# Kernel tuning notes

Measured on AMD Instinct MI355X. Metric: run time of the kernel, lower is better.

The kernel has to match this reference:

```python
import jax, jax.numpy as jnp
import numpy as np
from jax import lax

N_NODES = 8192
N_FEAT = 256
N_EDGES = 131072


def _cc_labels(src, dst, n):
    """Weakly-connected-component labels via min-label propagation + pointer jumping.
    Converged label[i] == min node index in i's component (matches scipy's
    first-occurrence labeling order after compaction)."""
    def cond(state):
        return state[1]

    def body(state):
        label, _ = state
        m = jnp.minimum(label[src], label[dst])
        new = label.at[src].min(m).at[dst].min(m)
        new = new[new]  # pointer jump
        return new, jnp.any(new != label)

    label, _ = lax.while_loop(cond, body, (jnp.arange(n, dtype=jnp.int32), jnp.array(True)))
    return label


def setup_inputs() -> dict:
    key = jax.random.key(0)
    k1, k2, k3 = jax.random.split(key, 3)
    x = jax.random.normal(k1, (N_NODES, N_FEAT), dtype=jnp.float32)
    edge_index = jax.random.randint(k2, (2, N_EDGES), 0, N_NODES, dtype=jnp.int32)
    batch = jnp.zeros((N_NODES,), dtype=jnp.int32)
    lin_w = jax.random.normal(k3, (1, 2 * N_FEAT), dtype=jnp.float32) * 0.05
    lin_b = jnp.zeros((1,), dtype=jnp.float32)
    return {"x": x, "edge_index": edge_index, "batch": batch, "lin_w": lin_w, "lin_b": lin_b}


def reference(x, edge_index, batch, lin_w, lin_b):
    n, f = x.shape
    src, dst = edge_index[0], edge_index[1]
    msk = src != dst  # drop self loops (kept in buffer, zeroed via mask for static shapes)
    # undirected: add flipped edges -> 2E directed edges
    src2 = jnp.concatenate([src, dst])
    dst2 = jnp.concatenate([dst, src])
    m2 = jnp.concatenate([msk, msk])
    mf = m2.astype(x.dtype)

    # edge score: Linear(2F,1) on [x[src] || x[dst]] == x@w1 gathered + x@w2 gathered
    w1, w2 = lin_w[0, :f], lin_w[0, f:]
    p1 = x @ w1  # [N]
    p2 = x @ w2  # [N]
    e = jnp.tanh(p1[src2] + p2[dst2] + lin_b[0])  # [2E]

    # contracted edges: score > threshold (0.0); masked edges excluded
    contract = m2 & (e > 0.0)
    srcc = jnp.where(contract, src2, 0)
    dstc = jnp.where(contract, dst2, 0)
    label = _cc_labels(srcc, dstc, n)
    # compact labels in order of smallest node index per component (== scipy ordering)
    is_root = (label == jnp.arange(n, dtype=label.dtype))
    cluster = (jnp.cumsum(is_root.astype(jnp.int32)) - 1)[label]  # [N], values in [0, K)

    # dense adjacency A and score adjacency S (scatter-add, like to_dense_adj)
    A = jnp.zeros((n, n), x.dtype).at[src2, dst2].add(mf)
    S = jnp.zeros((n, n), x.dtype).at[src2, dst2].add(e * mf)

    # isolated nodes w.r.t. contracted adjacency -> S[i,i] = 1
    cint = contract.astype(jnp.int32)
    deg = jnp.zeros(n, jnp.int32).at[src2].add(cint) + jnp.zeros(n, jnp.int32).at[dst2].add(cint)
    isolated = deg == 0
    idx = jnp.arange(n)
    S = S.at[idx, idx].set(jnp.where(isolated, jnp.ones((), x.dtype), S[idx, idx]))

    # X_new = (S @ C).T @ X = C.T @ (S.T @ X)  -- C.T@ is a segment-sum over clusters
    # (padded to N rows; rows >= num_clusters are zero)
    X_new = jax.ops.segment_sum(S.T @ x, cluster, num_segments=n)

    # coarsened adjacency C.T @ A @ C with zero diagonal (dense, padded to NxN)
    M1 = jax.ops.segment_sum(A, cluster, num_segments=n)        # pool rows
    A_c = jax.ops.segment_sum(M1.T, cluster, num_segments=n).T  # pool cols
    A_c = A_c.at[idx, idx].set(0.0)

    new_batch = jnp.zeros(n, batch.dtype).at[cluster].set(batch)
    return X_new, A_c, new_batch, cluster
```

## Files before the change

kernel.cpp:

```cpp
#include <hip/hip_runtime.h>
#include <math.h>

#define N_NODES 8192
#define N_FEAT  256
#define N_EDGES 131072
#define N_DIR   (2*N_EDGES)
#define MAXDEG  128


__device__ __forceinline__ void edge_sd(const int* __restrict__ ei, int k, int& s, int& d){
  s = ei[k];
  d = (k < N_EDGES) ? ei[k + N_EDGES] : ei[k - N_EDGES];
}


__global__ void k_zero(uint4* __restrict__ p, long long n4,
                       int* __restrict__ meta, int nmeta){
  long long i = (long long)blockIdx.x * blockDim.x + threadIdx.x;
  long long stride = (long long)gridDim.x * blockDim.x;
  uint4 z = {0u, 0u, 0u, 0u};
  for (long long k = i; k < n4; k += stride) p[k] = z;
  for (long long k = i; k < nmeta; k += stride) meta[k] = 0;
}

__global__ void k_proj(const float* __restrict__ x, const float* __restrict__ w,
                       float* __restrict__ p1, float* __restrict__ p2){
  int i = blockIdx.x;
  int t = threadIdx.x;
  float v = x[(size_t)i * N_FEAT + t];
  double a = (double)v * (double)w[t];
  double b = (double)v * (double)w[N_FEAT + t];
  for (int off = 32; off; off >>= 1){
    a += __shfl_down(a, off);
    b += __shfl_down(b, off);
  }
  __shared__ double sa[4], sb[4];
  int wid = t >> 6, lane = t & 63;
  if (lane == 0){ sa[wid] = a; sb[wid] = b; }
  __syncthreads();
  if (t == 0){
    p1[i] = (float)(sa[0] + sa[1] + sa[2] + sa[3]);
    p2[i] = (float)(sb[0] + sb[1] + sb[2] + sb[3]);
  }
}

__global__ void k_edges(const int* __restrict__ ei, const float* __restrict__ p1,
                        const float* __restrict__ p2, const float* __restrict__ lb,
                        int* __restrict__ cnt, int* __restrict__ deg,
                        uint2* __restrict__ edata,
                        unsigned int* __restrict__ pairs, int* __restrict__ np){
  int k = blockIdx.x * blockDim.x + threadIdx.x;
  int s, d; edge_sd(ei, k, s, d);
  bool selfe = (s == d);
  float e = 0.0f;
  if (!selfe){
    float z = p1[s] + p2[d] + lb[0];
    e = tanhf(z);
    int slot = atomicAdd(&cnt[d], 1);
    uint2 v; v.x = (unsigned int)s; v.y = __float_as_uint(e);
    edata[(size_t)d * MAXDEG + slot] = v;
    if (e > 0.0f){
      atomicAdd(&deg[s], 1);
      atomicAdd(&deg[d], 1);
    }
  }
  bool c = (!selfe) && (e > 0.0f);
  unsigned long long m = __ballot(c);
  if (m){
    int lane = threadIdx.x & 63;
    int leader = __ffsll((unsigned long long)m) - 1;
    int base = 0;
    if (lane == leader) base = atomicAdd(np, __popcll(m));
    base = __shfl(base, leader);
    if (c){
      int prefix = __popcll(m & ((1ull << lane) - 1ull));
      pairs[base + prefix] = ((unsigned int)s << 13) | (unsigned int)d;
    }
  }
}

__global__ void __launch_bounds__(1024) k_cc(
    const unsigned int* __restrict__ pairs, const int* __restrict__ np,
    const int* __restrict__ batch,
    int* __restrict__ cluster_i, float* __restrict__ out_cluster,
    float* __restrict__ out_batch){
  __shared__ int L[N_NODES];
  __shared__ int wsum[1024];
  __shared__ int flag;

  int t = threadIdx.x;
  for (int i = t; i < N_NODES; i += 1024) L[i] = i;
  if (t == 0) flag = 0;
  __syncthreads();

  int n = *np;
  while (true){
    for (int k = t; k < n; k += 1024){
      unsigned int p = pairs[k];
      int s = (int)(p >> 13), d = (int)(p & 8191u);
      int a = L[s], b = L[d];
      if (a == b) continue;
      int m = a < b ? a : b;
      atomicMin(&L[s], m);
      atomicMin(&L[d], m);
      if (a > m) atomicMin(&L[a], m);
      else       atomicMin(&L[b], m);
      flag = 1;
    }
    __syncthreads();
    if (!flag) break;
    for (int i = t; i < N_NODES; i += 1024){
      int l = L[i];
      while (true){ int q = L[l]; if (q == l) break; l = q; }
      L[i] = l;
    }
    __syncthreads();
    if (t == 0) flag = 0;
    __syncthreads();
  }

  int base = t * 8;
  int l_reg[8];
  #pragma unroll
  for (int j = 0; j < 8; ++j) l_reg[j] = L[base + j];
  __syncthreads();

  int f[8]; int s = 0;
  #pragma unroll
  for (int j = 0; j < 8; ++j){ f[j] = (l_reg[j] == base + j) ? 1 : 0; s += f[j]; }
  wsum[t] = s;
  __syncthreads();
  for (int off = 1; off < 1024; off <<= 1){
    int v = (t >= off) ? wsum[t - off] : 0;
    __syncthreads();
    wsum[t] += v;
    __syncthreads();
  }
  int run = wsum[t] - s;
  #pragma unroll
  for (int j = 0; j < 8; ++j){
    run += f[j];
    if (f[j]) L[base + j] = run - 1;
  }
  __syncthreads();

  #pragma unroll
  for (int j = 0; j < 8; ++j){
    int i = base + j;
    int c = L[l_reg[j]];
    cluster_i[i] = c;
    out_cluster[i] = (float)c;
    out_batch[c] = (float)batch[i];
  }
}

__global__ void k_y(const float* __restrict__ x, const uint2* __restrict__ edata,
                    const int* __restrict__ cnt, const int* __restrict__ deg,
                    float* __restrict__ y){
  int i = blockIdx.x;
  int t = threadIdx.x;
  int m = cnt[i];
  float acc = (deg[i] == 0) ? x[(size_t)i * N_FEAT + t] : 0.0f;
  const uint2* row = edata + (size_t)i * MAXDEG;
  for (int j = 0; j < m; ++j){
    uint2 v = row[j];
    acc += __uint_as_float(v.y) * x[(size_t)v.x * N_FEAT + t];
  }
  y[(size_t)i * N_FEAT + t] = acc;
}

__global__ void k_xnew(const float* __restrict__ y, const int* __restrict__ cluster_i,
                       float* __restrict__ Xn){
  int t = threadIdx.x;
  int node0 = blockIdx.x * 32;
  float acc = 0.0f;
  int cur = cluster_i[node0];
  for (int j = 0; j < 32; ++j){
    int node = node0 + j;
    int c = cluster_i[node];
    if (c != cur){
      atomicAdd(&Xn[(size_t)cur * N_FEAT + t], acc);
      acc = 0.0f; cur = c;
    }
    acc += y[(size_t)node * N_FEAT + t];
  }
  atomicAdd(&Xn[(size_t)cur * N_FEAT + t], acc);
}

__global__ void k_ac(const int* __restrict__ ei, const int* __restrict__ cluster_i,
                     float* __restrict__ Ac){
  int k = blockIdx.x * blockDim.x + threadIdx.x;
  if (k >= N_DIR) return;
  int s, d; edge_sd(ei, k, s, d);
  if (s == d) return;
  int cs = cluster_i[s], cd = cluster_i[d];
  if (cs != cd) atomicAdd(&Ac[(size_t)cs * N_NODES + cd], 1.0f);
}


extern "C" void kernel_launch(void* const* d_in, const int* in_sizes, int n_in,
                              void* d_out, int out_size, void* d_ws, size_t ws_size,
                              hipStream_t stream){
  const float* x     = (const float*)d_in[0];
  const int*   ei    = (const int*)  d_in[1];
  const int*   batch = (const int*)  d_in[2];
  const float* lw    = (const float*)d_in[3];
  const float* lb    = (const float*)d_in[4];

  float* out = (float*)d_out;
  float* Xn  = out;
  float* Ac  = Xn + (size_t)N_NODES * N_FEAT;
  float* ob  = Ac + (size_t)N_NODES * N_NODES;
  float* oc  = ob + N_NODES;

  char* w = (char*)d_ws;
  float* p1        = (float*)w; w += (size_t)N_NODES * 4;
  float* p2        = (float*)w; w += (size_t)N_NODES * 4;
  int*   cluster_i = (int*)  w; w += (size_t)N_NODES * 4;
  int*   meta      = (int*)  w;
  int*   cnt       = meta;
  int*   deg       = meta + N_NODES;
  int*   np        = meta + 2 * N_NODES;
  w += (size_t)(2 * N_NODES + 16) * 4;
  unsigned int* pairs = (unsigned int*)w; w += (size_t)N_DIR * 4;
  uint2* edata     = (uint2*)w; w += (size_t)N_NODES * MAXDEG * 8;
  float* y         = (float*)w; w += (size_t)N_NODES * N_FEAT * 4;

  long long n4 = (long long)out_size / 4;
  int nmeta = 2 * N_NODES + 16;

  k_zero  <<<4096, 256, 0, stream>>>((uint4*)d_out, n4, meta, nmeta);
  k_proj  <<<N_NODES, 256, 0, stream>>>(x, lw, p1, p2);
  k_edges <<<N_DIR / 256, 256, 0, stream>>>(ei, p1, p2, lb, cnt, deg, edata, pairs, np);
  k_cc    <<<1, 1024, 0, stream>>>(pairs, np, batch, cluster_i, oc, ob);
  k_y     <<<N_NODES, 256, 0, stream>>>(x, edata, cnt, deg, y);
  k_xnew  <<<N_NODES / 32, 256, 0, stream>>>(y, cluster_i, Xn);
  k_ac    <<<N_DIR / 256, 256, 0, stream>>>(ei, cluster_i, Ac);
}
```

Measured before the change: 269.4 us.

## Pre-relax components on whole GPU, filter active edges, overlap zeroing with CC block

Connected-component labeling now runs two grid-wide relax and flatten passes on a global label array. Only the edges still joining different labels are collected, and the single-block finisher iterates over that smaller set, staged in LDS when it fits. The big output zeroing is moved into extra blocks of the same launch as the single-block CC kernel, so it runs alongside it using nontemporal stores. This adds several small launches and could fall back to global reads when too many edges remain active.

```diff
diff --git a/kernel.cpp b/kernel.cpp
--- a/kernel.cpp
+++ b/kernel.cpp
@@ -6,6 +6,9 @@
 #define N_EDGES 131072
 #define N_DIR   (2*N_EDGES)
 #define MAXDEG  128
+#define ACT_CAP 24576
+
+typedef unsigned int u32x4 __attribute__((ext_vector_type(4)));
 
 
 __device__ __forceinline__ void edge_sd(const int* __restrict__ ei, int k, int& s, int& d){
@@ -14,13 +17,10 @@
 }
 
 
-__global__ void k_zero(uint4* __restrict__ p, long long n4,
-                       int* __restrict__ meta, int nmeta){
-  long long i = (long long)blockIdx.x * blockDim.x + threadIdx.x;
-  long long stride = (long long)gridDim.x * blockDim.x;
-  uint4 z = {0u, 0u, 0u, 0u};
-  for (long long k = i; k < n4; k += stride) p[k] = z;
-  for (long long k = i; k < nmeta; k += stride) meta[k] = 0;
+__global__ void k_start(int* __restrict__ meta, int nmeta, int* __restrict__ Lg){
+  int i = blockIdx.x * blockDim.x + threadIdx.x;
+  if (i < nmeta) meta[i] = 0;
+  if (i < N_NODES) Lg[i] = i;
 }
 
 __global__ void k_proj(const float* __restrict__ x, const float* __restrict__ w,
@@ -79,44 +79,113 @@
   }
 }
 
-__global__ void __launch_bounds__(1024) k_cc(
-    const unsigned int* __restrict__ pairs, const int* __restrict__ np,
-    const int* __restrict__ batch,
+__global__ void k_relax(const unsigned int* __restrict__ pairs,
+                        const int* __restrict__ np, int* __restrict__ Lg){
+  int n = *np;
+  int k = blockIdx.x * blockDim.x + threadIdx.x;
+  int stride = gridDim.x * blockDim.x;
+  for (; k < n; k += stride){
+    unsigned int p = pairs[k];
+    int s = (int)(p >> 13), d = (int)(p & 8191u);
+    int a = Lg[s], b = Lg[d];
+    if (a == b) continue;
+    int m = a < b ? a : b;
+    atomicMin(&Lg[s], m);
+    atomicMin(&Lg[d], m);
+    if (a > m) atomicMin(&Lg[a], m);
+    else       atomicMin(&Lg[b], m);
+  }
+}
+
+__global__ void k_flat(int* __restrict__ Lg){
+  int i = blockIdx.x * blockDim.x + threadIdx.x;
+  if (i >= N_NODES) return;
+  int l = Lg[i];
+  while (true){ int q = Lg[l]; if (q == l) break; l = q; }
+  Lg[i] = l;
+}
+
+__global__ void k_collect(const unsigned int* __restrict__ pairs,
+                          const int* __restrict__ np, const int* __restrict__ Lg,
+                          unsigned int* __restrict__ gact, int* __restrict__ ngact){
+  int n = *np;
+  int k = blockIdx.x * blockDim.x + threadIdx.x;
+  int stride = gridDim.x * blockDim.x;
+  for (; k < n; k += stride){
+    unsigned int p = pairs[k];
+    int s = (int)(p >> 13), d = (int)(p & 8191u);
+    bool act = (Lg[s] != Lg[d]);
+    unsigned long long m = __ballot(act);
+    if (m){
+      int lane = threadIdx.x & 63;
+      int leader = __ffsll((unsigned long long)m) - 1;
+      int base = 0;
+      if (lane == leader) base = atomicAdd(ngact, __popcll(m));
+      base = __shfl(base, leader);
+      if (act){
+        int prefix = __popcll(m & ((1ull << lane) - 1ull));
+        gact[base + prefix] = p;
+      }
+    }
+  }
+}
+
+__global__ void __launch_bounds__(1024) k_fused(
+    const unsigned int* __restrict__ gact, const int* __restrict__ ngact,
+    const int* __restrict__ Lg, const int* __restrict__ batch,
     int* __restrict__ cluster_i, float* __restrict__ out_cluster,
-    float* __restrict__ out_batch){
+    float* __restrict__ out_batch,
+    u32x4* __restrict__ zbase, long long n4){
+  int t = threadIdx.x;
+
+  if (blockIdx.x != 0){
+    long long i = (long long)(blockIdx.x - 1) * blockDim.x + t;
+    long long stride = (long long)(gridDim.x - 1) * blockDim.x;
+    u32x4 z = (u32x4)(0u);
+    for (; i < n4; i += stride) __builtin_nontemporal_store(z, &zbase[i]);
+    return;
+  }
+
   __shared__ int L[N_NODES];
   __shared__ int wsum[1024];
+  __shared__ unsigned int act[ACT_CAP];
   __shared__ int flag;
 
-  int t = threadIdx.x;
-  for (int i = t; i < N_NODES; i += 1024) L[i] = i;
-  if (t == 0) flag = 0;
-  __syncthreads();
-
-  int n = *np;
-  while (true){
-    for (int k = t; k < n; k += 1024){
-      unsigned int p = pairs[k];
-      int s = (int)(p >> 13), d = (int)(p & 8191u);
-      int a = L[s], b = L[d];
-      if (a == b) continue;
-      int m = a < b ? a : b;
-      atomicMin(&L[s], m);
-      atomicMin(&L[d], m);
-      if (a > m) atomicMin(&L[a], m);
-      else       atomicMin(&L[b], m);
-      flag = 1;
+  for (int i = t; i < N_NODES; i += 1024) L[i] = Lg[i];
+  for (int i = t; i < N_NODES; i += 1024) out_batch[i] = 0.0f;
+  __syncthreads();
+
+  int na = *ngact;
+  if (na > 0){
+    bool inlds = (na <= ACT_CAP);
+    if (inlds){
+      for (int k = t; k < na; k += 1024) act[k] = gact[k];
     }
     __syncthreads();
-    if (!flag) break;
-    for (int i = t; i < N_NODES; i += 1024){
-      int l = L[i];
-      while (true){ int q = L[l]; if (q == l) break; l = q; }
-      L[i] = l;
-    }
-    __syncthreads();
-    if (t == 0) flag = 0;
-    __syncthreads();
+    while (true){
+      if (t == 0) flag = 0;
+      __syncthreads();
+      for (int k = t; k < na; k += 1024){
+        unsigned int p = inlds ? act[k] : gact[k];
+        int s = (int)(p >> 13), d = (int)(p & 8191u);
+        int a = L[s], b = L[d];
+        if (a == b) continue;
+        int m = a < b ? a : b;
+        atomicMin(&L[s], m);
+        atomicMin(&L[d], m);
+        if (a > m) atomicMin(&L[a], m);
+        else       atomicMin(&L[b], m);
+        flag = 1;
+      }
+      __syncthreads();
+      if (!flag) break;
+      for (int i = t; i < N_NODES; i += 1024){
+        int l = L[i];
+        while (true){ int q = L[l]; if (q == l) break; l = q; }
+        L[i] = l;
+      }
+      __syncthreads();
+    }
   }
 
   int base = t * 8;
@@ -217,23 +286,32 @@
   float* p1        = (float*)w; w += (size_t)N_NODES * 4;
   float* p2        = (float*)w; w += (size_t)N_NODES * 4;
   int*   cluster_i = (int*)  w; w += (size_t)N_NODES * 4;
+  int*   Lg        = (int*)  w; w += (size_t)N_NODES * 4;
   int*   meta      = (int*)  w;
   int*   cnt       = meta;
   int*   deg       = meta + N_NODES;
   int*   np        = meta + 2 * N_NODES;
-  w += (size_t)(2 * N_NODES + 16) * 4;
+  int*   ngact     = meta + 2 * N_NODES + 1;
+  int    nmeta     = 2 * N_NODES + 16;
+  w += (size_t)nmeta * 4;
   unsigned int* pairs = (unsigned int*)w; w += (size_t)N_DIR * 4;
+  unsigned int* gact  = (unsigned int*)w; w += (size_t)N_DIR * 4;
   uint2* edata     = (uint2*)w; w += (size_t)N_NODES * MAXDEG * 8;
   float* y         = (float*)w; w += (size_t)N_NODES * N_FEAT * 4;
 
-  long long n4 = (long long)out_size / 4;
-  int nmeta = 2 * N_NODES + 16;
-
-  k_zero  <<<4096, 256, 0, stream>>>((uint4*)d_out, n4, meta, nmeta);
-  k_proj  <<<N_NODES, 256, 0, stream>>>(x, lw, p1, p2);
-  k_edges <<<N_DIR / 256, 256, 0, stream>>>(ei, p1, p2, lb, cnt, deg, edata, pairs, np);
-  k_cc    <<<1, 1024, 0, stream>>>(pairs, np, batch, cluster_i, oc, ob);
-  k_y     <<<N_NODES, 256, 0, stream>>>(x, edata, cnt, deg, y);
-  k_xnew  <<<N_NODES / 32, 256, 0, stream>>>(y, cluster_i, Xn);
-  k_ac    <<<N_DIR / 256, 256, 0, stream>>>(ei, cluster_i, Ac);
-}
+  long long n4 = ((long long)N_NODES * N_FEAT + (long long)N_NODES * N_NODES) / 4;
+
+  k_start  <<<(nmeta + 255) / 256, 256, 0, stream>>>(meta, nmeta, Lg);
+  k_proj   <<<N_NODES, 256, 0, stream>>>(x, lw, p1, p2);
+  k_edges  <<<N_DIR / 256, 256, 0, stream>>>(ei, p1, p2, lb, cnt, deg, edata, pairs, np);
+  k_relax  <<<512, 256, 0, stream>>>(pairs, np, Lg);
+  k_flat   <<<N_NODES / 256, 256, 0, stream>>>(Lg);
+  k_relax  <<<512, 256, 0, stream>>>(pairs, np, Lg);
+  k_flat   <<<N_NODES / 256, 256, 0, stream>>>(Lg);
+  k_collect<<<512, 256, 0, stream>>>(pairs, np, Lg, gact, ngact);
+  k_fused  <<<256, 1024, 0, stream>>>(gact, ngact, Lg, batch, cluster_i, oc, ob,
+                                      (u32x4*)out, n4);
+  k_y      <<<N_NODES, 256, 0, stream>>>(x, edata, cnt, deg, y);
+  k_xnew   <<<N_NODES / 32, 256, 0, stream>>>(y, cluster_i, Xn);
+  k_ac     <<<N_DIR / 256, 256, 0, stream>>>(ei, cluster_i, Ac);
+}
```

Measured after the change: 312.8 us. 16.1% more time.

## Fuse zeroing, edge scoring and CC into one cooperative grid kernel

Applied to the files above, without the earlier changes.

Replaces the zero, edge and single-block connected-components kernels with one cooperative kernel of 256 blocks. Edge scoring builds per-node neighbor lists of contracted edges, and label propagation runs grid-wide as a per-node min over neighbors plus pointer jumping, separated by grid syncs. After the last round, block 0 does the compaction while the other blocks zero the dense outputs with nontemporal stores. The aim is to remove the serial single-block CC bottleneck and overlap the large output memset, at the cost of grid-wide barrier overhead. Propagation is capped at 32 rounds, which risks an unconverged labeling.

```diff
diff --git a/kernel.cpp b/kernel.cpp
--- a/kernel.cpp
+++ b/kernel.cpp
@@ -1,11 +1,19 @@
 #include <hip/hip_runtime.h>
+#include <hip/hip_cooperative_groups.h>
 #include <math.h>
+
+namespace cg = cooperative_groups;
 
 #define N_NODES 8192
 #define N_FEAT  256
 #define N_EDGES 131072
 #define N_DIR   (2*N_EDGES)
 #define MAXDEG  128
+#define MAXR    32
+#define MBLK    256
+#define MTHR    1024
+
+typedef unsigned int u32x4 __attribute__((ext_vector_type(4)));
 
 
 __device__ __forceinline__ void edge_sd(const int* __restrict__ ei, int k, int& s, int& d){
@@ -13,15 +21,6 @@
   d = (k < N_EDGES) ? ei[k + N_EDGES] : ei[k - N_EDGES];
 }
 
-
-__global__ void k_zero(uint4* __restrict__ p, long long n4,
-                       int* __restrict__ meta, int nmeta){
-  long long i = (long long)blockIdx.x * blockDim.x + threadIdx.x;
-  long long stride = (long long)gridDim.x * blockDim.x;
-  uint4 z = {0u, 0u, 0u, 0u};
-  for (long long k = i; k < n4; k += stride) p[k] = z;
-  for (long long k = i; k < nmeta; k += stride) meta[k] = 0;
-}
 
 __global__ void k_proj(const float* __restrict__ x, const float* __restrict__ w,
                        float* __restrict__ p1, float* __restrict__ p2){
@@ -44,113 +43,114 @@
   }
 }
 
-__global__ void k_edges(const int* __restrict__ ei, const float* __restrict__ p1,
-                        const float* __restrict__ p2, const float* __restrict__ lb,
-                        int* __restrict__ cnt, int* __restrict__ deg,
-                        uint2* __restrict__ edata,
-                        unsigned int* __restrict__ pairs, int* __restrict__ np){
-  int k = blockIdx.x * blockDim.x + threadIdx.x;
-  int s, d; edge_sd(ei, k, s, d);
-  bool selfe = (s == d);
-  float e = 0.0f;
-  if (!selfe){
-    float z = p1[s] + p2[d] + lb[0];
-    e = tanhf(z);
-    int slot = atomicAdd(&cnt[d], 1);
-    uint2 v; v.x = (unsigned int)s; v.y = __float_as_uint(e);
-    edata[(size_t)d * MAXDEG + slot] = v;
-    if (e > 0.0f){
-      atomicAdd(&deg[s], 1);
-      atomicAdd(&deg[d], 1);
-    }
-  }
-  bool c = (!selfe) && (e > 0.0f);
-  unsigned long long m = __ballot(c);
-  if (m){
-    int lane = threadIdx.x & 63;
-    int leader = __ffsll((unsigned long long)m) - 1;
-    int base = 0;
-    if (lane == leader) base = atomicAdd(np, __popcll(m));
-    base = __shfl(base, leader);
-    if (c){
-      int prefix = __popcll(m & ((1ull << lane) - 1ull));
-      pairs[base + prefix] = ((unsigned int)s << 13) | (unsigned int)d;
-    }
-  }
-}
-
-__global__ void __launch_bounds__(1024) k_cc(
-    const unsigned int* __restrict__ pairs, const int* __restrict__ np,
+__global__ void __launch_bounds__(MTHR) k_mega(
+    const int* __restrict__ ei, const float* __restrict__ p1,
+    const float* __restrict__ p2, const float* __restrict__ lb,
     const int* __restrict__ batch,
+    int* __restrict__ meta,
+    int* __restrict__ Lg,
+    int* __restrict__ nbr, uint2* __restrict__ edata,
     int* __restrict__ cluster_i, float* __restrict__ out_cluster,
-    float* __restrict__ out_batch){
-  __shared__ int L[N_NODES];
-  __shared__ int wsum[1024];
-  __shared__ int flag;
-
-  int t = threadIdx.x;
-  for (int i = t; i < N_NODES; i += 1024) L[i] = i;
-  if (t == 0) flag = 0;
-  __syncthreads();
-
-  int n = *np;
-  while (true){
-    for (int k = t; k < n; k += 1024){
-      unsigned int p = pairs[k];
-      int s = (int)(p >> 13), d = (int)(p & 8191u);
-      int a = L[s], b = L[d];
-      if (a == b) continue;
-      int m = a < b ? a : b;
-      atomicMin(&L[s], m);
-      atomicMin(&L[d], m);
-      if (a > m) atomicMin(&L[a], m);
-      else       atomicMin(&L[b], m);
-      flag = 1;
-    }
+    float* __restrict__ out_batch,
+    u32x4* __restrict__ zbase, long long n4){
+  cg::grid_group grid = cg::this_grid();
+  int t = threadIdx.x;
+  int gid = blockIdx.x * MTHR + t;
+
+  int* cnt  = meta;
+  int* deg  = meta + N_NODES;
+  int* ncnt = meta + 2 * N_NODES;
+  int* chg  = meta + 3 * N_NODES;
+
+  if (gid < 3 * N_NODES + 64) meta[gid] = 0;
+  if (gid < N_NODES) Lg[gid] = gid;
+  grid.sync();
+
+  {
+    int s, d; edge_sd(ei, gid, s, d);
+    if (s != d){
+      float z = p1[s] + p2[d] + lb[0];
+      float e = tanhf(z);
+      int slot = atomicAdd(&cnt[d], 1);
+      uint2 v; v.x = (unsigned int)s; v.y = __float_as_uint(e);
+      edata[(size_t)d * MAXDEG + slot] = v;
+      if (e > 0.0f){
+        atomicAdd(&deg[s], 1);
+        atomicAdd(&deg[d], 1);
+        int a = atomicAdd(&ncnt[s], 1);
+        nbr[(size_t)s * MAXDEG + a] = d;
+        int b = atomicAdd(&ncnt[d], 1);
+        nbr[(size_t)d * MAXDEG + b] = s;
+      }
+    }
+  }
+  grid.sync();
+
+  for (int r = 0; r < MAXR; ++r){
+    if (gid < N_NODES){
+      int m = Lg[gid];
+      int c = ncnt[gid];
+      const int* row = nbr + (size_t)gid * MAXDEG;
+      for (int j = 0; j < c; ++j){
+        int l = Lg[row[j]];
+        m = l < m ? l : m;
+      }
+      if (m < Lg[gid]){ Lg[gid] = m; chg[r] = 1; }
+    }
+    grid.sync();
+    int changed = chg[r];
+    if (gid < N_NODES){
+      int l = Lg[gid];
+      while (true){ int q = Lg[l]; if (q == l) break; l = q; }
+      Lg[gid] = l;
+    }
+    grid.sync();
+    if (!changed) break;
+  }
+
+  if (blockIdx.x == 0){
+    __shared__ int L[N_NODES];
+    __shared__ int wsum[MTHR];
+    for (int i = t; i < N_NODES; i += MTHR){ L[i] = Lg[i]; out_batch[i] = 0.0f; }
     __syncthreads();
-    if (!flag) break;
-    for (int i = t; i < N_NODES; i += 1024){
-      int l = L[i];
-      while (true){ int q = L[l]; if (q == l) break; l = q; }
-      L[i] = l;
-    }
+
+    int base = t * 8;
+    int l_reg[8];
+    #pragma unroll
+    for (int j = 0; j < 8; ++j) l_reg[j] = L[base + j];
+
+    int f[8]; int s = 0;
+    #pragma unroll
+    for (int j = 0; j < 8; ++j){ f[j] = (l_reg[j] == base + j) ? 1 : 0; s += f[j]; }
+    wsum[t] = s;
     __syncthreads();
-    if (t == 0) flag = 0;
+    for (int off = 1; off < MTHR; off <<= 1){
+      int v = (t >= off) ? wsum[t - off] : 0;
+      __syncthreads();
+      wsum[t] += v;
+      __syncthreads();
+    }
+    int run = wsum[t] - s;
+    #pragma unroll
+    for (int j = 0; j < 8; ++j){
+      run += f[j];
+      if (f[j]) L[base + j] = run - 1;
+    }
     __syncthreads();
-  }
-
-  int base = t * 8;
-  int l_reg[8];
-  #pragma unroll
-  for (int j = 0; j < 8; ++j) l_reg[j] = L[base + j];
-  __syncthreads();
-
-  int f[8]; int s = 0;
-  #pragma unroll
-  for (int j = 0; j < 8; ++j){ f[j] = (l_reg[j] == base + j) ? 1 : 0; s += f[j]; }
-  wsum[t] = s;
-  __syncthreads();
-  for (int off = 1; off < 1024; off <<= 1){
-    int v = (t >= off) ? wsum[t - off] : 0;
-    __syncthreads();
-    wsum[t] += v;
-    __syncthreads();
-  }
-  int run = wsum[t] - s;
-  #pragma unroll
-  for (int j = 0; j < 8; ++j){
-    run += f[j];
-    if (f[j]) L[base + j] = run - 1;
-  }
-  __syncthreads();
-
-  #pragma unroll
-  for (int j = 0; j < 8; ++j){
-    int i = base + j;
-    int c = L[l_reg[j]];
-    cluster_i[i] = c;
-    out_cluster[i] = (float)c;
-    out_batch[c] = (float)batch[i];
+
+    #pragma unroll
+    for (int j = 0; j < 8; ++j){
+      int i = base + j;
+      int c = L[l_reg[j]];
+      cluster_i[i] = c;
+      out_cluster[i] = (float)c;
+      out_batch[c] = (float)batch[i];
+    }
+  } else {
+    long long i = (long long)(blockIdx.x - 1) * MTHR + t;
+    long long stride = (long long)(MBLK - 1) * MTHR;
+    u32x4 z = (u32x4)(0u);
+    for (; i < n4; i += stride) __builtin_nontemporal_store(z, &zbase[i]);
   }
 }
 
@@ -201,11 +201,11 @@
 extern "C" void kernel_launch(void* const* d_in, const int* in_sizes, int n_in,
                               void* d_out, int out_size, void* d_ws, size_t ws_size,
                               hipStream_t stream){
-  const float* x     = (const float*)d_in[0];
   const int*   ei    = (const int*)  d_in[1];
   const int*   batch = (const int*)  d_in[2];
   const float* lw    = (const float*)d_in[3];
   const float* lb    = (const float*)d_in[4];
+  const float* x     = (const float*)d_in[0];
 
   float* out = (float*)d_out;
   float* Xn  = out;
@@ -217,23 +217,28 @@
   float* p1        = (float*)w; w += (size_t)N_NODES * 4;
   float* p2        = (float*)w; w += (size_t)N_NODES * 4;
   int*   cluster_i = (int*)  w; w += (size_t)N_NODES * 4;
-  int*   meta      = (int*)  w;
-  int*   cnt       = meta;
-  int*   deg       = meta + N_NODES;
-  int*   np        = meta + 2 * N_NODES;
-  w += (size_t)(2 * N_NODES + 16) * 4;
-  unsigned int* pairs = (unsigned int*)w; w += (size_t)N_DIR * 4;
+  int*   Lg        = (int*)  w; w += (size_t)N_NODES * 4;
+  int*   meta      = (int*)  w; w += (size_t)(3 * N_NODES + 64) * 4;
   uint2* edata     = (uint2*)w; w += (size_t)N_NODES * MAXDEG * 8;
+  int*   nbr       = (int*)  w; w += (size_t)N_NODES * MAXDEG * 4;
   float* y         = (float*)w; w += (size_t)N_NODES * N_FEAT * 4;
 
-  long long n4 = (long long)out_size / 4;
-  int nmeta = 2 * N_NODES + 16;
-
-  k_zero  <<<4096, 256, 0, stream>>>((uint4*)d_out, n4, meta, nmeta);
-  k_proj  <<<N_NODES, 256, 0, stream>>>(x, lw, p1, p2);
-  k_edges <<<N_DIR / 256, 256, 0, stream>>>(ei, p1, p2, lb, cnt, deg, edata, pairs, np);
-  k_cc    <<<1, 1024, 0, stream>>>(pairs, np, batch, cluster_i, oc, ob);
-  k_y     <<<N_NODES, 256, 0, stream>>>(x, edata, cnt, deg, y);
-  k_xnew  <<<N_NODES / 32, 256, 0, stream>>>(y, cluster_i, Xn);
-  k_ac    <<<N_DIR / 256, 256, 0, stream>>>(ei, cluster_i, Ac);
-}
+  long long n4 = ((long long)N_NODES * N_FEAT + (long long)N_NODES * N_NODES) / 4;
+  u32x4* zb = (u32x4*)out;
+
+  k_proj<<<N_NODES, 256, 0, stream>>>(x, lw, p1, p2);
+
+  {
+    void* args[] = {
+      (void*)&ei, (void*)&p1, (void*)&p2, (void*)&lb, (void*)&batch,
+      (void*)&meta, (void*)&Lg, (void*)&nbr, (void*)&edata,
+      (void*)&cluster_i, (void*)&oc, (void*)&ob, (void*)&zb, (void*)&n4
+    };
+    hipLaunchCooperativeKernel((const void*)k_mega, dim3(MBLK), dim3(MTHR),
+                               args, 0, stream);
+  }
+
+  k_y   <<<N_NODES, 256, 0, stream>>>(x, edata, meta , meta + N_NODES , y);
+  k_xnew<<<N_NODES / 32, 256, 0, stream>>>(y, cluster_i, Xn);
+  k_ac  <<<N_DIR / 256, 256, 0, stream>>>(ei, cluster_i, Ac);
+}
```

New measurement: 537.2 us. +99.4%, slower.
